# Optimization experiments

Hardware: AMD Instinct MI355X
Metric: run time of the kernel (lower is better)

Reference implementation:

```python
import jax, jax.numpy as jnp
import numpy as np

B, C, N, QK, VC, S = 64, 64, 256, 8, 32, 16
EPS = 1e-5
SCALE = float(np.sqrt(QK))  # qk_channel ** 0.5


def _bn(x, p):
    # eval-mode BatchNorm1d over [B, C, N]; p = [gamma, beta, mean, var]
    g, b, m, v = p
    return (x - m[None, :, None]) * (g * jax.lax.rsqrt(v + EPS))[None, :, None] + b[None, :, None]


def _conv1x1(w, x, b=None):
    y = jnp.einsum('oc,bcn->bon', w, x)
    return y if b is None else y + b[None, :, None]


def setup_inputs() -> dict:
    key = jax.random.key(0)
    ks = jax.random.split(key, 16)

    def w(k, o, i):
        return jax.random.normal(k, (o, i), jnp.float32) * (1.0 / np.sqrt(i))

    def bn_p(k, c):
        k1, k2, k3, k4 = jax.random.split(k, 4)
        return jnp.stack([
            jax.random.uniform(k1, (c,), jnp.float32) + 0.5,   # gamma
            jax.random.normal(k2, (c,), jnp.float32) * 0.1,    # beta
            jax.random.normal(k3, (c,), jnp.float32) * 0.1,    # running mean
            jax.random.uniform(k4, (c,), jnp.float32) + 0.5,   # running var (>0)
        ])

    x = jax.random.normal(ks[0], (B, C, N), jnp.float32)
    stroke_idx = jax.random.randint(ks[1], (B, N), 0, S, jnp.int32)
    stroke_idx = stroke_idx.at[:, -1].set(S - 1)  # guarantee max == S-1

    ga_q_w = w(ks[2], QK, C)
    sa_q_w = w(ks[3], QK, C)
    inp = {
        'x': x,
        'stroke_idx': stroke_idx,
        'n_strokes': S,
        'ga_q_w': ga_q_w,
        'ga_k_w': ga_q_w.copy(),  # k initialized as clone of q in source
        'ga_v_w': w(ks[4], VC, C),
        'ga_v_b': jax.random.normal(ks[5], (VC,), jnp.float32) * 0.01,
        'ga_bn_p': bn_p(ks[6], VC),
        'ga_lb_w': w(ks[7], VC, C),
        'ga_lb_bn_p': bn_p(ks[8], VC),
        'sa_q_w': sa_q_w,
        'sa_k_w': sa_q_w.copy(),
        'sa_v_w': w(ks[9], VC, C),
        'sa_v_b': jax.random.normal(ks[10], (VC,), jnp.float32) * 0.01,
        'sa_bn_p': bn_p(ks[11], VC),
        'sa_lb_w': w(ks[12], VC, C),
        'sa_lb_bn_p': bn_p(ks[13], VC),
        'mlp_w1': w(ks[14], 4 * C, C),
        'mlp_bn1_p': bn_p(jax.random.fold_in(key, 100), 4 * C),
        'mlp_w2': w(ks[15], C, 4 * C),
        'mlp_bn2_p': bn_p(jax.random.fold_in(key, 101), C),
    }
    return inp


def _ga_block(x, qw, kw, vw, vb):
    q = jnp.einsum('oc,bcn->bno', qw, x)                 # [B,N,QK]
    k = jnp.einsum('oc,bcn->bon', kw, x)                 # [B,QK,N]
    v = jnp.einsum('oc,bcn->bno', vw, x) + vb[None, None, :]  # [B,N,VC]
    attn = jax.nn.softmax(jnp.einsum('bno,bom->bnm', q, k) / SCALE, axis=-1)
    return jnp.einsum('bnm,bmv->bvn', attn, v)           # [B,VC,N]


def _sa_block(x, stroke_idx, n_strokes, qw, kw, vw, vb):
    q = jnp.einsum('oc,bcn->bno', qw, x)
    k = jnp.einsum('oc,bcn->bon', kw, x)
    v = jnp.einsum('oc,bcn->bno', vw, x) + vb[None, None, :]
    base = jnp.einsum('bno,bom->bnm', q, k) / SCALE      # [B,N,N]
    # per-stroke additive mask: 0 where stroke == i else 1e-6 (as in source)
    masks = jnp.where(stroke_idx[None, :, :] == jnp.arange(n_strokes)[:, None, None],
                      0.0, 1e-6).astype(base.dtype)       # [S,B,N]
    energy = (base[None] + masks[:, :, None, :]) * 10.0   # [S,B,N,N]
    attn = jax.nn.softmax(energy, axis=-1)
    # sum over strokes fused into the contraction
    return jnp.einsum('sbnm,bmv->bvn', attn, v)           # [B,VC,N]


def reference(x, stroke_idx, n_strokes, ga_q_w, ga_k_w, ga_v_w, ga_v_b, ga_bn_p,
              ga_lb_w, ga_lb_bn_p, sa_q_w, sa_k_w, sa_v_w, sa_v_b, sa_bn_p,
              sa_lb_w, sa_lb_bn_p, mlp_w1, mlp_bn1_p, mlp_w2, mlp_bn2_p):
    f_ga = _bn(_ga_block(x, ga_q_w, ga_k_w, ga_v_w, ga_v_b), ga_bn_p) \
         + _bn(_conv1x1(ga_lb_w, x), ga_lb_bn_p)
    f_sa = _bn(_sa_block(x, stroke_idx, n_strokes, sa_q_w, sa_k_w, sa_v_w, sa_v_b), sa_bn_p) \
         + _bn(_conv1x1(sa_lb_w, x), sa_lb_bn_p)
    f = jnp.concatenate([f_ga, f_sa], axis=1)            # [B,C,N]
    h = jax.nn.relu(_bn(_conv1x1(mlp_w1, f), mlp_bn1_p))  # [B,4C,N]
    f_mlp = _bn(_conv1x1(mlp_w2, h), mlp_bn2_p)           # [B,C,N]
    return jax.nn.relu(f_mlp + f)
```

## Files before the change

### kernel.cpp

```cpp
#include <hip/hip_runtime.h>
#include <math.h>


#define EPS    1e-5f
#define LOG2E  1.4426950408889634f

#define OFF_QGA 0u
#define OFF_KGA 131072u
#define OFF_VGA 262144u
#define OFF_QSA 786432u
#define OFF_KSA 917504u
#define OFF_VSA 1048576u
#define OFF_F   1572864u
#define OFF_H   2621440u

__global__ __launch_bounds__(512) void k_proj(
    const float* __restrict__ x,
    const float* __restrict__ gaq, const float* __restrict__ gak,
    const float* __restrict__ gav, const float* __restrict__ gavb,
    const float* __restrict__ galb, const float* __restrict__ galbbn,
    const float* __restrict__ saq, const float* __restrict__ sak,
    const float* __restrict__ sav, const float* __restrict__ savb,
    const float* __restrict__ salb, const float* __restrict__ salbbn,
    float* ws)
{
    __shared__ float O2[160][65];
    const int lane = threadIdx.x & 63;
    const int wvu  = __builtin_amdgcn_readfirstlane((int)(threadIdx.x >> 6));
    const int b    = blockIdx.x >> 2;
    const int n0   = (blockIdx.x & 3) << 6;
    const int p0g  = blockIdx.x << 6;

    float xr[64];
    const float* xb = x + (size_t)(b * 64) * 256 + n0 + lane;
    #pragma unroll
    for (int c = 0; c < 64; ++c) xr[c] = xb[c * 256];

    for (int i = 0; i < 20; ++i) {
        const int slot = wvu * 20 + i;
        const float* wr; float mul = 1.f, add = 0.f;
        if (slot < 8)        { wr = gaq + slot * 64; }
        else if (slot < 16)  { wr = gak + (slot - 8) * 64; }
        else if (slot < 48)  { int vc = slot - 16; wr = gav + vc * 64; add = gavb[vc]; }
        else if (slot < 56)  { wr = saq + (slot - 48) * 64; }
        else if (slot < 64)  { wr = sak + (slot - 56) * 64; }
        else if (slot < 96)  { int vc = slot - 64; wr = sav + vc * 64; add = savb[vc]; }
        else if (slot < 128) { int vc = slot - 96; wr = galb + vc * 64;
                               float s = galbbn[vc] * rsqrtf(galbbn[96 + vc] + EPS);
                               mul = s; add = galbbn[32 + vc] - galbbn[64 + vc] * s; }
        else                 { int vc = slot - 128; wr = salb + vc * 64;
                               float s = salbbn[vc] * rsqrtf(salbbn[96 + vc] + EPS);
                               mul = s; add = salbbn[32 + vc] - salbbn[64 + vc] * s; }
        float acc = 0.f;
        #pragma unroll
        for (int c = 0; c < 64; ++c) acc = fmaf(wr[c], xr[c], acc);
        O2[slot][lane] = acc * mul + add;
    }
    __syncthreads();

    for (int t = threadIdx.x; t < 2560; t += 512) {
        int u, rb, l; unsigned g;
        if (t < 128)       { u = t;        rb = 0;   l = 1; g = OFF_QGA; }
        else if (t < 256)  { u = t - 128;  rb = 8;   l = 1; g = OFF_KGA; }
        else if (t < 768)  { u = t - 256;  rb = 16;  l = 3; g = OFF_VGA; }
        else if (t < 896)  { u = t - 768;  rb = 48;  l = 1; g = OFF_QSA; }
        else if (t < 1024) { u = t - 896;  rb = 56;  l = 1; g = OFF_KSA; }
        else if (t < 1536) { u = t - 1024; rb = 64;  l = 3; g = OFF_VSA; }
        else               { u = t - 1536; rb = 96;  l = 4; g = OFF_F;   }
        const int p    = u >> l;
        const int off4 = u & ((1 << l) - 1);
        const int row  = rb + off4 * 4;
        float4 v;
        v.x = O2[row + 0][p]; v.y = O2[row + 1][p];
        v.z = O2[row + 2][p]; v.w = O2[row + 3][p];
        *(float4*)(ws + g + (size_t)(p0g + p) * (4u << l) + off4 * 4) = v;
    }
}

__global__ __launch_bounds__(512, 4) void k_attn(
    const float* __restrict__ wsr, const float* __restrict__ gabnp,
    const float* __restrict__ sabnp, float* F)
{
    __shared__ __align__(16) float KL[2076];
    __shared__ __align__(16) float VL[8220];
    const int which = blockIdx.x >> 8;
    const int bb    = blockIdx.x & 255;
    const int b     = bb >> 2;
    const int q0    = (bb & 3) << 6;
    const unsigned ro = which ? 786432u : 0u;
    const float* Q = wsr + OFF_QGA + ro;
    const float* K = wsr + OFF_KGA + ro + (size_t)b * 2048;
    const float* V = wsr + OFF_VGA + ro + (size_t)b * 8192;
    const float* bnp = which ? sabnp : gabnp;
    const float factor   = which ? 3.5355339059327378f : 0.35355339059327378f;
    const float outscale = which ? 16.f : 1.f;
    const int   choff    = which << 5;

    const int lane = threadIdx.x & 63;
    const int w    = (int)(threadIdx.x >> 6);
    const int qr   = lane >> 3;
    const int g    = lane & 7;
    const int p    = b * 256 + q0 + (w << 3) + qr;

    float4 qa = *(const float4*)(Q + (size_t)p * 8);
    float4 qb = *(const float4*)(Q + (size_t)p * 8 + 4);

    {
        const int t = (int)threadIdx.x;
        {
            const float4 v = *(const float4*)(K + t * 4);
            const int m = t >> 1, h = t & 1;
            *(float4*)&KL[m * 8 + (m >> 5) * 4 + h * 4] = v;
        }
        #pragma unroll
        for (int k2 = 0; k2 < 4; ++k2) {
            const int u = t + k2 * 512;
            const float4 v = *(const float4*)(V + u * 4);
            const int m = u >> 3, j4 = u & 7;
            *(float4*)&VL[m * 32 + (m >> 5) * 4 + j4 * 4] = v;
        }
    }
    __syncthreads();

    const float fl = factor * LOG2E;
    qa.x *= fl; qa.y *= fl; qa.z *= fl; qa.w *= fl;
    qb.x *= fl; qb.y *= fl; qb.z *= fl; qb.w *= fl;

    const int kb0 = g * 260;
    float s[32];
    float M = -1e30f;
    #pragma unroll
    for (int i = 0; i < 32; ++i) {
        const float4 k0 = *(const float4*)&KL[kb0 + i * 8];
        const float4 k1 = *(const float4*)&KL[kb0 + i * 8 + 4];
        s[i] = qa.x * k0.x + qa.y * k0.y + qa.z * k0.z + qa.w * k0.w
             + qb.x * k1.x + qb.y * k1.y + qb.z * k1.z + qb.w * k1.w;
        M = fmaxf(M, s[i]);
    }

    const int vb0 = g * 1028;
    float Z = 0.f;
    float acc[32];
    #pragma unroll
    for (int j = 0; j < 32; ++j) acc[j] = 0.f;
    #pragma unroll
    for (int i = 0; i < 32; ++i) {
        const float pv = exp2f(s[i] - M);
        Z += pv;
        const float* vr = &VL[vb0 + i * 32];
        #pragma unroll
        for (int j4 = 0; j4 < 8; ++j4) {
            const float4 vv = *(const float4*)(vr + (j4 << 2));
            acc[j4 * 4 + 0] = fmaf(pv, vv.x, acc[j4 * 4 + 0]);
            acc[j4 * 4 + 1] = fmaf(pv, vv.y, acc[j4 * 4 + 1]);
            acc[j4 * 4 + 2] = fmaf(pv, vv.z, acc[j4 * 4 + 2]);
            acc[j4 * 4 + 3] = fmaf(pv, vv.w, acc[j4 * 4 + 3]);
        }
    }

    float Mx = M;
    Mx = fmaxf(Mx, __shfl_xor(Mx, 1));
    Mx = fmaxf(Mx, __shfl_xor(Mx, 2));
    Mx = fmaxf(Mx, __shfl_xor(Mx, 4));
    const float cw = exp2f(M - Mx);
    Z *= cw;
    #pragma unroll
    for (int j = 0; j < 32; ++j) acc[j] *= cw;
    Z += __shfl_xor(Z, 1);
    Z += __shfl_xor(Z, 2);
    Z += __shfl_xor(Z, 4);
    float r16[16];
    #pragma unroll
    for (int t = 0; t < 16; ++t) {
        float snd = (g & 4) ? acc[t] : acc[16 + t];
        float rcv = __shfl_xor(snd, 4);
        r16[t] = ((g & 4) ? acc[16 + t] : acc[t]) + rcv;
    }
    float r8[8];
    #pragma unroll
    for (int t = 0; t < 8; ++t) {
        float snd = (g & 2) ? r16[t] : r16[8 + t];
        float rcv = __shfl_xor(snd, 2);
        r8[t] = ((g & 2) ? r16[8 + t] : r16[t]) + rcv;
    }
    float a4[4];
    #pragma unroll
    for (int t = 0; t < 4; ++t) {
        float snd = (g & 1) ? r8[t] : r8[4 + t];
        float rcv = __shfl_xor(snd, 1);
        a4[t] = ((g & 1) ? r8[4 + t] : r8[t]) + rcv;
    }

    const int vc0 = g << 2;
    const float4 ga4 = *(const float4*)(bnp + vc0);
    const float4 be4 = *(const float4*)(bnp + 32 + vc0);
    const float4 mn4 = *(const float4*)(bnp + 64 + vc0);
    const float4 va4 = *(const float4*)(bnp + 96 + vc0);
    const float iz = 1.f / Z;
    float* fp = F + (size_t)p * 64 + choff + vc0;
    float4 old = *(const float4*)fp;
    float4 o;
    {
        float gs = ga4.x * rsqrtf(va4.x + EPS);
        o.x = old.x + a4[0] * iz * gs * outscale + (be4.x - mn4.x * gs);
    }
    {
        float gs = ga4.y * rsqrtf(va4.y + EPS);
        o.y = old.y + a4[1] * iz * gs * outscale + (be4.y - mn4.y * gs);
    }
    {
        float gs = ga4.z * rsqrtf(va4.z + EPS);
        o.z = old.z + a4[2] * iz * gs * outscale + (be4.z - mn4.z * gs);
    }
    {
        float gs = ga4.w * rsqrtf(va4.w + EPS);
        o.w = old.w + a4[3] * iz * gs * outscale + (be4.w - mn4.w * gs);
    }
    *(float4*)fp = o;
}

__global__ __launch_bounds__(256) void k_mlp1(
    const float* __restrict__ Fin, const float* __restrict__ w1,
    const float* __restrict__ bn1, float* __restrict__ H)
{
    __shared__ __align__(16) float wL[64][68];
    const int jg = blockIdx.x & 3;
    const int nt = (blockIdx.x >> 2) & 7;
    const int b  = blockIdx.x >> 5;
    const int j0 = jg << 6;
    const int n0 = nt << 5;
    for (int t = threadIdx.x; t < 4096; t += 256) {
        int jj = t >> 6, c = t & 63;
        wL[jj][c] = w1[(j0 + jj) * 64 + c];
    }
    __syncthreads();
    const int lane = threadIdx.x & 63;
    const int wq = __builtin_amdgcn_readfirstlane((int)(threadIdx.x >> 6));
    const int j  = j0 + lane;
    const int pbase = b * 256 + n0 + wq * 8;
    const float* f0 = Fin + (size_t)pbase * 64;
    float acc[8] = {0.f,0.f,0.f,0.f,0.f,0.f,0.f,0.f};
    #pragma unroll
    for (int c4 = 0; c4 < 16; ++c4) {
        float4 wv = *(const float4*)&wL[lane][c4 * 4];
        #pragma unroll
        for (int r = 0; r < 8; ++r) {
            float4 fv = *(const float4*)&f0[r * 64 + c4 * 4];
            acc[r] += wv.x * fv.x + wv.y * fv.y + wv.z * fv.z + wv.w * fv.w;
        }
    }
    const float gg = bn1[j], be = bn1[256 + j], mn = bn1[512 + j], va = bn1[768 + j];
    const float s    = gg * rsqrtf(va + EPS);
    const float bias = be - mn * s;
    #pragma unroll
    for (int r = 0; r < 8; ++r)
        H[(size_t)(pbase + r) * 256 + j] = fmaxf(acc[r] * s + bias, 0.f);
}

__global__ __launch_bounds__(256) void k_mlp2(
    const float* __restrict__ H, const float* __restrict__ w2,
    const float* __restrict__ bn2, const float* __restrict__ Fin,
    float* __restrict__ out)
{
    __shared__ __align__(16) float w2L[64][268];
    __shared__ float OT[64][33];
    const int b   = blockIdx.x >> 3;
    const int nw  = (blockIdx.x & 7) << 5;
    for (int t = threadIdx.x; t < 16384; t += 256) {
        w2L[t >> 8][t & 255] = w2[t];
    }
    __syncthreads();
    const int lane = threadIdx.x & 63;
    const int wq = __builtin_amdgcn_readfirstlane((int)(threadIdx.x >> 6));
    const float g = bn2[lane], be = bn2[64 + lane], mn = bn2[128 + lane], va = bn2[192 + lane];
    const float s    = g * rsqrtf(va + EPS);
    const float bias = be - mn * s;
    for (int g2 = 0; g2 < 2; ++g2) {
        const int nl = wq * 8 + g2 * 4;
        const int pb = b * 256 + nw + nl;
        const float* h0 = H + (size_t)pb * 256;
        float acc[4] = {0.f,0.f,0.f,0.f};
        for (int j4 = 0; j4 < 64; ++j4) {
            float4 wv = *(const float4*)&w2L[lane][j4 * 4];
            #pragma unroll
            for (int r = 0; r < 4; ++r) {
                float4 hv = *(const float4*)&h0[r * 256 + j4 * 4];
                acc[r] += wv.x * hv.x + wv.y * hv.y + wv.z * hv.z + wv.w * hv.w;
            }
        }
        #pragma unroll
        for (int r = 0; r < 4; ++r) {
            float f = Fin[(size_t)(pb + r) * 64 + lane];
            OT[lane][nl + r] = fmaxf(acc[r] * s + bias + f, 0.f);
        }
    }
    __syncthreads();
    for (int t = threadIdx.x; t < 512; t += 256) {
        int c = t >> 3, j4 = (t & 7) << 2;
        float4 v;
        v.x = OT[c][j4]; v.y = OT[c][j4 + 1]; v.z = OT[c][j4 + 2]; v.w = OT[c][j4 + 3];
        *(float4*)(out + (size_t)(b * 64 + c) * 256 + nw + j4) = v;
    }
}

extern "C" void kernel_launch(void* const* d_in, const int* in_sizes, int n_in,
                              void* d_out, int out_size, void* d_ws, size_t ws_size,
                              hipStream_t stream) {
    const float* x      = (const float*)d_in[0];
    const float* gaq    = (const float*)d_in[3];
    const float* gak    = (const float*)d_in[4];
    const float* gav    = (const float*)d_in[5];
    const float* gavb   = (const float*)d_in[6];
    const float* gabnp  = (const float*)d_in[7];
    const float* galb   = (const float*)d_in[8];
    const float* galbbn = (const float*)d_in[9];
    const float* saq    = (const float*)d_in[10];
    const float* sak    = (const float*)d_in[11];
    const float* sav    = (const float*)d_in[12];
    const float* savb   = (const float*)d_in[13];
    const float* sabnp  = (const float*)d_in[14];
    const float* salb   = (const float*)d_in[15];
    const float* salbbn = (const float*)d_in[16];
    const float* w1     = (const float*)d_in[17];
    const float* bn1    = (const float*)d_in[18];
    const float* w2     = (const float*)d_in[19];
    const float* bn2    = (const float*)d_in[20];
    float* ws   = (float*)d_ws;
    float* outp = (float*)d_out;

    k_proj<<<dim3(256), dim3(512), 0, stream>>>(
        x, gaq, gak, gav, gavb, galb, galbbn,
        saq, sak, sav, savb, salb, salbbn, ws);

    k_attn<<<dim3(512), dim3(512), 0, stream>>>(ws, gabnp, sabnp, ws + OFF_F);

    k_mlp1<<<dim3(2048), dim3(256), 0, stream>>>(ws + OFF_F, w1, bn1, ws + OFF_H);
    k_mlp2<<<dim3(512),  dim3(256), 0, stream>>>(ws + OFF_H, w2, bn2, ws + OFF_F, outp);
}
```

Before: 169.4 us.

## Split mlp2 output channels across two blocks to raise parallelism and cut LDS

```diff
diff --git a/kernel.cpp b/kernel.cpp
--- a/kernel.cpp
+++ b/kernel.cpp
@@ -257,49 +257,59 @@
         H[(size_t)(pbase + r) * 256 + j] = fmaxf(acc[r] * s + bias, 0.f);
 }
 
-__global__ __launch_bounds__(256) void k_mlp2(
+__global__ __launch_bounds__(256, 4) void k_mlp2(
     const float* __restrict__ H, const float* __restrict__ w2,
     const float* __restrict__ bn2, const float* __restrict__ Fin,
     float* __restrict__ out)
 {
-    __shared__ __align__(16) float w2L[64][268];
-    __shared__ float OT[64][33];
-    const int b   = blockIdx.x >> 3;
-    const int nw  = (blockIdx.x & 7) << 5;
-    for (int t = threadIdx.x; t < 16384; t += 256) {
-        w2L[t >> 8][t & 255] = w2[t];
-    }
-    __syncthreads();
+    __shared__ __align__(16) float w2L[32 * 268];
+    __shared__ float OT[32][33];
+    const int chh = blockIdx.x & 1;
+    const int nw  = ((blockIdx.x >> 1) & 7) << 5;
+    const int b   = blockIdx.x >> 4;
+    const int ch0 = chh << 5;
+
+    for (int t = threadIdx.x; t < 2048; t += 256) {
+        const int r = t >> 6, c4 = (t & 63) << 2;
+        const float4 v = *(const float4*)(w2 + (size_t)(ch0 + r) * 256 + c4);
+        *(float4*)&w2L[r * 268 + c4] = v;
+    }
+    __syncthreads();
+
     const int lane = threadIdx.x & 63;
-    const int wq = __builtin_amdgcn_readfirstlane((int)(threadIdx.x >> 6));
-    const float g = bn2[lane], be = bn2[64 + lane], mn = bn2[128 + lane], va = bn2[192 + lane];
+    const int wq   = __builtin_amdgcn_readfirstlane((int)(threadIdx.x >> 6));
+    const int c    = lane & 31;
+    const int ph   = lane >> 5;
+    const int cg   = ch0 + c;
+
+    const int pb = b * 256 + nw + wq * 8 + ph * 4;
+    const float* h0 = H + (size_t)pb * 256;
+    float acc[4] = {0.f, 0.f, 0.f, 0.f};
+    #pragma unroll 4
+    for (int j4 = 0; j4 < 64; ++j4) {
+        const float4 wv = *(const float4*)&w2L[c * 268 + (j4 << 2)];
+        #pragma unroll
+        for (int r = 0; r < 4; ++r) {
+            const float4 hv = *(const float4*)&h0[r * 256 + (j4 << 2)];
+            acc[r] += wv.x * hv.x + wv.y * hv.y + wv.z * hv.z + wv.w * hv.w;
+        }
+    }
+    const float g = bn2[cg], be = bn2[64 + cg], mn = bn2[128 + cg], va = bn2[192 + cg];
     const float s    = g * rsqrtf(va + EPS);
     const float bias = be - mn * s;
-    for (int g2 = 0; g2 < 2; ++g2) {
-        const int nl = wq * 8 + g2 * 4;
-        const int pb = b * 256 + nw + nl;
-        const float* h0 = H + (size_t)pb * 256;
-        float acc[4] = {0.f,0.f,0.f,0.f};
-        for (int j4 = 0; j4 < 64; ++j4) {
-            float4 wv = *(const float4*)&w2L[lane][j4 * 4];
-            #pragma unroll
-            for (int r = 0; r < 4; ++r) {
-                float4 hv = *(const float4*)&h0[r * 256 + j4 * 4];
-                acc[r] += wv.x * hv.x + wv.y * hv.y + wv.z * hv.z + wv.w * hv.w;
-            }
-        }
-        #pragma unroll
-        for (int r = 0; r < 4; ++r) {
-            float f = Fin[(size_t)(pb + r) * 64 + lane];
-            OT[lane][nl + r] = fmaxf(acc[r] * s + bias + f, 0.f);
-        }
-    }
-    __syncthreads();
-    for (int t = threadIdx.x; t < 512; t += 256) {
-        int c = t >> 3, j4 = (t & 7) << 2;
+    #pragma unroll
+    for (int r = 0; r < 4; ++r) {
+        const float f = Fin[(size_t)(pb + r) * 64 + cg];
+        OT[c][wq * 8 + ph * 4 + r] = fmaxf(acc[r] * s + bias + f, 0.f);
+    }
+    __syncthreads();
+    {
+        const int t  = (int)threadIdx.x;
+        const int cc = t >> 3, j4 = (t & 7) << 2;
         float4 v;
-        v.x = OT[c][j4]; v.y = OT[c][j4 + 1]; v.z = OT[c][j4 + 2]; v.w = OT[c][j4 + 3];
-        *(float4*)(out + (size_t)(b * 64 + c) * 256 + nw + j4) = v;
+        v.x = OT[cc][j4]; v.y = OT[cc][j4 + 1];
+        v.z = OT[cc][j4 + 2]; v.w = OT[cc][j4 + 3];
+        *(float4*)(out + (size_t)(b * 64 + ch0 + cc) * 256 + nw + j4) = v;
     }
 }
 
@@ -335,5 +345,5 @@
     k_attn<<<dim3(512), dim3(512), 0, stream>>>(ws, gabnp, sabnp, ws + OFF_F);
 
     k_mlp1<<<dim3(2048), dim3(256), 0, stream>>>(ws + OFF_F, w1, bn1, ws + OFF_H);
-    k_mlp2<<<dim3(512),  dim3(256), 0, stream>>>(ws + OFF_H, w2, bn2, ws + OFF_F, outp);
-}
+    k_mlp2<<<dim3(1024), dim3(256), 0, stream>>>(ws + OFF_H, w2, bn2, ws + OFF_F, outp);
+}
```

New measurement: 178.3 us. 1.05x slower.
